# Performance work log

Hardware: AMD Instinct MI355X
Metric: run time of the kernel (lower is better)

The kernel has to match this reference:

```python
import jax, jax.numpy as jnp
import numpy as np

N_NODES = 100000
N_EDGES = 1600000
D_FEAT = 128
HIDDEN = 128
N_CLASSES = 40


def setup_inputs() -> dict:
    key = jax.random.key(0)
    ks = jax.random.split(key, 8)
    s = 1.0 / np.sqrt(HIDDEN)
    return {
        "x": jax.random.normal(ks[0], (N_NODES, D_FEAT), dtype=jnp.float32),
        "edge_index": jax.random.randint(ks[1], (2, N_EDGES), 0, N_NODES, dtype=jnp.int64),
        "w1a": jax.random.normal(ks[2], (D_FEAT, HIDDEN), dtype=jnp.float32) * s,
        "b1a": jnp.zeros((HIDDEN,), dtype=jnp.float32),
        "w1b": jax.random.normal(ks[3], (HIDDEN, HIDDEN), dtype=jnp.float32) * s,
        "b1b": jnp.zeros((HIDDEN,), dtype=jnp.float32),
        "w2a": jax.random.normal(ks[4], (HIDDEN, HIDDEN), dtype=jnp.float32) * s,
        "b2a": jnp.zeros((HIDDEN,), dtype=jnp.float32),
        "w2b": jax.random.normal(ks[5], (HIDDEN, HIDDEN), dtype=jnp.float32) * s,
        "b2b": jnp.zeros((HIDDEN,), dtype=jnp.float32),
        "wfc": jax.random.normal(ks[6], (HIDDEN, N_CLASSES), dtype=jnp.float32) * s,
        "bfc": jnp.zeros((N_CLASSES,), dtype=jnp.float32),
    }


def _gin_conv(x, src, dst, wa, ba, wb, bb):
    # sum-aggregate neighbor features: agg[i] = sum_{(j->i) in E} x[j]
    agg = jax.ops.segment_sum(x[src], dst, num_segments=N_NODES)
    h = x + agg  # eps = 0 (PyG GINConv default)
    h = jax.nn.relu(h @ wa + ba)
    return h @ wb + bb


def reference(x, edge_index, w1a, b1a, w1b, b1b, w2a, b2a, w2b, b2b, wfc, bfc):
    src, dst = edge_index[0], edge_index[1]
    h = jax.nn.relu(_gin_conv(x, src, dst, w1a, b1a, w1b, b1b))
    # dropout is identity at inference
    h = jax.nn.relu(_gin_conv(h, src, dst, w2a, b2a, w2b, b2b))
    logits = h @ wfc + bfc
    return jax.nn.log_softmax(logits, axis=1)
```

## Files before the change

kernel.cpp:

```cpp
#include <hip/hip_runtime.h>
#include <hip/hip_bf16.h>

#define NNODES 100000
#define NEDGES 1600000
#define DF 128
#define NC 40
#define NCP 48
#define NB 196
#define CH 4096
#define GEMM_BLOCKS 512
#define GEMM_WAVES (GEMM_BLOCKS * 4)
#define ZROW NNODES

typedef __bf16 bf16x8 __attribute__((ext_vector_type(8)));
typedef float f32x4 __attribute__((ext_vector_type(4)));
typedef float f32x2 __attribute__((ext_vector_type(2)));

__device__ __forceinline__ unsigned short f2bf(float f) {
    unsigned int u = __builtin_bit_cast(unsigned int, f);
    u = (u + 0x7FFFu + ((u >> 16) & 1u)) >> 16;
    return (unsigned short)u;
}
__device__ __forceinline__ float bf2f(unsigned short s) {
    unsigned int u = ((unsigned int)s) << 16;
    return __builtin_bit_cast(float, u);
}
__device__ __forceinline__ float bfLo(unsigned int u) {
    return __builtin_bit_cast(float, u << 16);
}
__device__ __forceinline__ float bfHi(unsigned int u) {
    return __builtin_bit_cast(float, u & 0xFFFF0000u);
}
__device__ __forceinline__ f32x2 up2(unsigned int u) {
    return (f32x2){bfLo(u), bfHi(u)};
}

__global__ void k_detect(const unsigned int* __restrict__ ei32,
                         const unsigned int* __restrict__ x32,
                         int* __restrict__ flags,
                         int* __restrict__ binCnt) {
    __shared__ unsigned int rOr[256];
    __shared__ int rCnt[256];
    for (int i = threadIdx.x; i < NB; i += 256) binCnt[i] = 0;
    unsigned int o = 0; int c = 0;
    for (int i = threadIdx.x; i < 1024; i += 256) o |= ei32[2 * i + 1];
    for (int i = threadIdx.x; i < 4096; i += 256) {
        unsigned int e = (x32[i] >> 7) & 0xFFu;
        c += (e >= 100u && e <= 140u) ? 1 : 0;
    }
    rOr[threadIdx.x] = o; rCnt[threadIdx.x] = c;
    __syncthreads();
    for (int s = 128; s; s >>= 1) {
        if ((int)threadIdx.x < s) {
            rOr[threadIdx.x] |= rOr[threadIdx.x + s];
            rCnt[threadIdx.x] += rCnt[threadIdx.x + s];
        }
        __syncthreads();
    }
    if (threadIdx.x == 0) {
        flags[0] = (rOr[0] == 0u) ? 1 : 0;
        flags[1] = (rCnt[0] > 2457) ? 1 : 0;
    }
}

__device__ __forceinline__ int ldIdx(const void* ei, int flag64, int i) {
    return flag64 ? (int)((const long long*)ei)[i] : ((const int*)ei)[i];
}

__global__ __launch_bounds__(256) void k_cvt_feat(const void* __restrict__ src,
                                                  const int* __restrict__ flags,
                                                  unsigned short* __restrict__ dst) {
    int i = blockIdx.x * 256 + threadIdx.x;
    if (flags[1]) {
        ((uint4*)dst)[i] = ((const uint4*)src)[i];
    } else {
        uint4 a = ((const uint4*)src)[2 * i];
        uint4 b = ((const uint4*)src)[2 * i + 1];
        auto pk = [](unsigned int lo, unsigned int hi) -> unsigned int {
            return ((unsigned int)f2bf(__builtin_bit_cast(float, hi)) << 16) |
                   f2bf(__builtin_bit_cast(float, lo));
        };
        uint4 r;
        r.x = pk(a.x, a.y);
        r.y = pk(a.z, a.w);
        r.z = pk(b.x, b.y);
        r.w = pk(b.z, b.w);
        ((uint4*)dst)[i] = r;
    }
}

__global__ __launch_bounds__(256) void k_wprep(const void* w1a, const void* w1b,
                                               const void* w2a, const void* w2b,
                                               const void* wfc,
                                               const void* b1a, const void* b1b,
                                               const void* b2a, const void* b2b,
                                               const void* bfc,
                                               const int* __restrict__ flags,
                                               unsigned short* __restrict__ wAll,
                                               float* __restrict__ bAll,
                                               unsigned short* __restrict__ pad0,
                                               unsigned short* __restrict__ pad1) {
    int idx = blockIdx.x * 256 + threadIdx.x;
    int bf = flags[1];
    auto ldf = [&](const void* p, int i) -> float {
        return bf ? bf2f(((const unsigned short*)p)[i]) : ((const float*)p)[i];
    };
    if (idx < 65536) {
        int wi = idx >> 14, r = idx & 16383;
        int n = r >> 7, k = r & 127;
        const void* s = (wi == 0) ? w1a : (wi == 1) ? w1b : (wi == 2) ? w2a : w2b;
        wAll[idx] = f2bf(ldf(s, k * 128 + n));
    } else if (idx < 65536 + NCP * 128) {
        int r = idx - 65536;
        int n = r >> 7, k = r & 127;
        wAll[idx] = (n < NC) ? f2bf(ldf(wfc, k * NC + n)) : (unsigned short)0;
    } else if (idx < 65536 + NCP * 128 + 512 + NC) {
        int r = idx - (65536 + NCP * 128);
        const void* s; int i;
        if (r < 128)      { s = b1a; i = r; }
        else if (r < 256) { s = b1b; i = r - 128; }
        else if (r < 384) { s = b2a; i = r - 256; }
        else if (r < 512) { s = b2b; i = r - 384; }
        else              { s = bfc; i = r - 512; }
        bAll[r] = ldf(s, i);
    } else if (idx < 65536 + NCP * 128 + 512 + NC + 256) {
        pad0[idx - (65536 + NCP * 128 + 512 + NC)] = 0;
    } else if (idx < 65536 + NCP * 128 + 512 + NC + 512) {
        pad1[idx - (65536 + NCP * 128 + 512 + NC + 256)] = 0;
    }
}

__global__ __launch_bounds__(256) void k_bincount(const void* __restrict__ ei,
                                                  const int* __restrict__ flags,
                                                  int* __restrict__ binCnt) {
    __shared__ int l[NB];
    int t = threadIdx.x;
    int f64 = flags[0];
    for (int i = t; i < NB; i += 256) l[i] = 0;
    __syncthreads();
    int base = blockIdx.x * CH;
#pragma unroll
    for (int k = 0; k < CH / 256; k++) {
        int e = base + k * 256 + t;
        if (e < NEDGES) atomicAdd(&l[ldIdx(ei, f64, NEDGES + e) >> 9], 1);
    }
    __syncthreads();
    for (int i = t; i < NB; i += 256)
        if (l[i]) atomicAdd(&binCnt[i], l[i]);
}

__global__ __launch_bounds__(256) void k_binscan(const int* __restrict__ binCnt,
                                                 int* __restrict__ binOfs,
                                                 int* __restrict__ binCur) {
    __shared__ int sh[256];
    int t = threadIdx.x;
    int v = (t < NB) ? binCnt[t] : 0;
    sh[t] = v;
    __syncthreads();
    for (int off = 1; off < 256; off <<= 1) {
        int x = (t >= off) ? sh[t - off] : 0;
        __syncthreads();
        sh[t] += x;
        __syncthreads();
    }
    if (t < NB) {
        binOfs[t + 1] = sh[t];
        binCur[t] = sh[t] - v;
    }
    if (t == 0) binOfs[0] = 0;
}

__global__ __launch_bounds__(256) void k_binscatter(const void* __restrict__ ei,
                                                    const int* __restrict__ flags,
                                                    int* __restrict__ binCur,
                                                    int2* __restrict__ ebin) {
    __shared__ int lcnt[NB], lbase[NB], lofs[NB];
    int t = threadIdx.x;
    int f64 = flags[0];
    for (int i = t; i < NB; i += 256) lcnt[i] = 0;
    __syncthreads();
    int base = blockIdx.x * CH;
    int2 ed[CH / 256];
    int bn[CH / 256];
#pragma unroll
    for (int k = 0; k < CH / 256; k++) {
        int e = base + k * 256 + t;
        if (e < NEDGES) {
            ed[k].x = ldIdx(ei, f64, e);
            ed[k].y = ldIdx(ei, f64, NEDGES + e);
            bn[k] = ed[k].y >> 9;
            atomicAdd(&lcnt[bn[k]], 1);
        } else bn[k] = -1;
    }
    __syncthreads();
    if (t < NB) {
        int c = lcnt[t];
        lbase[t] = c ? atomicAdd(&binCur[t], c) : 0;
        lofs[t] = 0;
    }
    __syncthreads();
#pragma unroll
    for (int k = 0; k < CH / 256; k++) {
        if (bn[k] >= 0) {
            int p = lbase[bn[k]] + atomicAdd(&lofs[bn[k]], 1);
            ebin[p] = ed[k];
        }
    }
}

__global__ __launch_bounds__(256) void k_binfill(const int2* __restrict__ ebin,
                                                 const int* __restrict__ binOfs,
                                                 int* __restrict__ rowptr,
                                                 int* __restrict__ perm) {
    __shared__ int deg[512], lptr[512], ssum[256];
    int b = blockIdx.x, t = threadIdx.x;
    int n0 = b << 9;
    int nn = NNODES - n0; if (nn > 512) nn = 512;
    int e0 = binOfs[b], e1 = binOfs[b + 1];
    deg[t] = 0; deg[t + 256] = 0;
    __syncthreads();
    for (int e = e0 + t; e < e1; e += 256)
        atomicAdd(&deg[ebin[e].y - n0], 1);
    __syncthreads();
    int d0 = deg[2 * t], d1 = deg[2 * t + 1];
    int s = d0 + d1;
    ssum[t] = s;
    __syncthreads();
    for (int off = 1; off < 256; off <<= 1) {
        int x = (t >= off) ? ssum[t - off] : 0;
        __syncthreads();
        ssum[t] += x;
        __syncthreads();
    }
    int ex = ssum[t] - s;
    lptr[2 * t] = ex;
    lptr[2 * t + 1] = ex + d0;
    if (2 * t < nn)     rowptr[n0 + 2 * t] = e0 + ex;
    if (2 * t + 1 < nn) rowptr[n0 + 2 * t + 1] = e0 + ex + d0;
    if (b == NB - 1 && t == 0) rowptr[NNODES] = e1;
    deg[2 * t] = 0; deg[2 * t + 1] = 0;
    __syncthreads();
    for (int e = e0 + t; e < e1; e += 256) {
        int2 ed = ebin[e];
        int d = ed.y - n0;
        int pos = e0 + lptr[d] + atomicAdd(&deg[d], 1);
        perm[pos] = ed.x;
    }
}

__device__ __forceinline__ void accu(f32x2* acc, uint4 u) {
    acc[0] += up2(u.x);
    acc[1] += up2(u.y);
    acc[2] += up2(u.z);
    acc[3] += up2(u.w);
}

template <int S>
__device__ __forceinline__ void gslots(const int* __restrict__ perm, const uint4* __restrict__ F,
                                       int j, int je, int g, int c, f32x2* acc) {
    int pm[S];
#pragma unroll
    for (int k = 0; k < S; k++) pm[k] = perm[j + 4 * k + g];
#pragma unroll
    for (int k = 0; k < S; k++)
        if (j + 4 * k + g >= je) pm[k] = ZROW;
    uint4 u[S];
#pragma unroll
    for (int k = 0; k < S; k++) u[k] = F[pm[k] * 16 + c];
#pragma unroll
    for (int k = 0; k < S; k++) accu(acc, u[k]);
}

__global__ __launch_bounds__(256) void k_gather(const unsigned short* __restrict__ feat,
                                                const unsigned short* __restrict__ x,
                                                const int* __restrict__ rowptr,
                                                const int* __restrict__ perm,
                                                unsigned short* __restrict__ out) {
    int wave = threadIdx.x >> 6, lane = threadIdx.x & 63;
    int i = blockIdx.x * 4 + wave;
    int g = lane >> 4, c = lane & 15;
    const uint4* F = (const uint4*)feat;

    uint4 xv = ((const uint4*)x)[i * 16 + c];
    int jb = rowptr[i], je = rowptr[i + 1];

    f32x2 acc[4];
#pragma unroll
    for (int k = 0; k < 4; k++) acc[k] = (f32x2){0.f, 0.f};

    int j = jb;
    while (je - j > 24) {
        int s0 = perm[j + g], s1 = perm[j + 4 + g];
        int s2 = perm[j + 8 + g], s3 = perm[j + 12 + g];
        uint4 u0 = F[s0 * 16 + c];
        uint4 u1 = F[s1 * 16 + c];
        uint4 u2 = F[s2 * 16 + c];
        uint4 u3 = F[s3 * 16 + c];
        accu(acc, u0); accu(acc, u1); accu(acc, u2); accu(acc, u3);
        j += 16;
    }
    int deg = je - j;
    if (deg > 16)      gslots<6>(perm, F, j, je, g, c, acc);
    else if (deg > 8)  gslots<4>(perm, F, j, je, g, c, acc);
    else if (deg > 0)  gslots<2>(perm, F, j, je, g, c, acc);

#pragma unroll
    for (int k = 0; k < 4; k++) {
        acc[k][0] += __shfl_xor(acc[k][0], 16);
        acc[k][1] += __shfl_xor(acc[k][1], 16);
        acc[k][0] += __shfl_xor(acc[k][0], 32);
        acc[k][1] += __shfl_xor(acc[k][1], 32);
    }

    acc[0] += up2(xv.x);
    acc[1] += up2(xv.y);
    acc[2] += up2(xv.z);
    acc[3] += up2(xv.w);

    if (g == 0) {
        uint4 r;
        r.x = ((unsigned int)f2bf(acc[0][1]) << 16) | f2bf(acc[0][0]);
        r.y = ((unsigned int)f2bf(acc[1][1]) << 16) | f2bf(acc[1][0]);
        r.z = ((unsigned int)f2bf(acc[2][1]) << 16) | f2bf(acc[2][0]);
        r.w = ((unsigned int)f2bf(acc[3][1]) << 16) | f2bf(acc[3][0]);
        ((uint4*)out)[i * 16 + c] = r;
    }
}

__global__ __launch_bounds__(256, 2) void k_gemm_rb(const unsigned short* __restrict__ A,
                                                    const unsigned short* __restrict__ WT,
                                                    const float* __restrict__ bias,
                                                    unsigned short* __restrict__ out) {
    int gw = blockIdx.x * 4 + (threadIdx.x >> 6);
    int lane = threadIdx.x & 63;
    int m = lane & 15, quad = lane >> 4;

    bf16x8 bfr[8][4];
#pragma unroll
    for (int nt = 0; nt < 8; nt++) {
        const unsigned short* Bb = WT + (nt * 16 + m) * DF + quad * 8;
#pragma unroll
        for (int ks = 0; ks < 4; ks++)
            bfr[nt][ks] = *(const bf16x8*)(Bb + ks * 32);
    }
    float bv[8];
#pragma unroll
    for (int nt = 0; nt < 8; nt++) bv[nt] = bias[nt * 16 + m];

    for (int tile = gw; tile < NNODES / 16; tile += GEMM_WAVES) {
        int r0 = tile * 16;
        const unsigned short* Ab = A + (r0 + m) * DF + quad * 8;
        bf16x8 a[4];
#pragma unroll
        for (int ks = 0; ks < 4; ks++) a[ks] = *(const bf16x8*)(Ab + ks * 32);

        f32x4 acc[8];
#pragma unroll
        for (int nt = 0; nt < 8; nt++) acc[nt] = (f32x4){0.f, 0.f, 0.f, 0.f};
#pragma unroll
        for (int nt = 0; nt < 8; nt++)
#pragma unroll
            for (int ks = 0; ks < 4; ks++)
                acc[nt] = __builtin_amdgcn_mfma_f32_16x16x32_bf16(a[ks], bfr[nt][ks], acc[nt], 0, 0, 0);

#pragma unroll
        for (int nt = 0; nt < 8; nt++) {
            int col = nt * 16 + m;
#pragma unroll
            for (int reg = 0; reg < 4; reg++) {
                int row = r0 + quad * 4 + reg;
                float v = acc[nt][reg] + bv[nt];
                if (v < 0.f) v = 0.f;
                out[row * DF + col] = f2bf(v);
            }
        }
    }
}

__global__ __launch_bounds__(256, 2) void k_fc_rb(const unsigned short* __restrict__ A,
                                                  const unsigned short* __restrict__ WfcT,
                                                  const float* __restrict__ bfc,
                                                  const int* __restrict__ flags,
                                                  void* __restrict__ out) {
    int gw = blockIdx.x * 4 + (threadIdx.x >> 6);
    int lane = threadIdx.x & 63;
    int m = lane & 15, quad = lane >> 4;
    bool valid2 = (m < 8);
    int obf = flags[1];

    bf16x8 bfr[3][4];
#pragma unroll
    for (int nt = 0; nt < 3; nt++) {
        const unsigned short* Bb = WfcT + (nt * 16 + m) * DF + quad * 8;
#pragma unroll
        for (int ks = 0; ks < 4; ks++)
            bfr[nt][ks] = *(const bf16x8*)(Bb + ks * 32);
    }
    float bv0 = bfc[m], bv1 = bfc[16 + m];
    float bv2 = valid2 ? bfc[32 + m] : 0.f;

    for (int tile = gw; tile < NNODES / 16; tile += GEMM_WAVES) {
        int r0 = tile * 16;
        const unsigned short* Ab = A + (r0 + m) * DF + quad * 8;
        bf16x8 a[4];
#pragma unroll
        for (int ks = 0; ks < 4; ks++) a[ks] = *(const bf16x8*)(Ab + ks * 32);

        f32x4 acc[3];
#pragma unroll
        for (int nt = 0; nt < 3; nt++) acc[nt] = (f32x4){0.f, 0.f, 0.f, 0.f};
#pragma unroll
        for (int nt = 0; nt < 3; nt++)
#pragma unroll
            for (int ks = 0; ks < 4; ks++)
                acc[nt] = __builtin_amdgcn_mfma_f32_16x16x32_bf16(a[ks], bfr[nt][ks], acc[nt], 0, 0, 0);

#pragma unroll
        for (int reg = 0; reg < 4; reg++) {
            float v0 = acc[0][reg] + bv0;
            float v1 = acc[1][reg] + bv1;
            float v2 = valid2 ? (acc[2][reg] + bv2) : -3.0e38f;
            float mx = fmaxf(fmaxf(v0, v1), v2);
#pragma unroll
            for (int off = 1; off < 16; off <<= 1) mx = fmaxf(mx, __shfl_xor(mx, off, 16));
            float e = __expf(v0 - mx) + __expf(v1 - mx) + (valid2 ? __expf(v2 - mx) : 0.f);
#pragma unroll
            for (int off = 1; off < 16; off <<= 1) e += __shfl_xor(e, off, 16);
            float l = mx + __logf(e);
            int row = r0 + quad * 4 + reg;
            if (obf) {
                unsigned short* o = (unsigned short*)out + row * NC;
                o[m] = f2bf(v0 - l);
                o[16 + m] = f2bf(v1 - l);
                if (valid2) o[32 + m] = f2bf(v2 - l);
            } else {
                float* o = (float*)out + row * NC;
                o[m] = v0 - l;
                o[16 + m] = v1 - l;
                if (valid2) o[32 + m] = v2 - l;
            }
        }
    }
}

extern "C" void kernel_launch(void* const* d_in, const int* in_sizes, int n_in,
                              void* d_out, int out_size, void* d_ws, size_t ws_size,
                              hipStream_t stream) {
    const void* x   = d_in[0];
    const void* ei  = d_in[1];
    const void* w1a = d_in[2];
    const void* b1a = d_in[3];
    const void* w1b = d_in[4];
    const void* b1b = d_in[5];
    const void* w2a = d_in[6];
    const void* b2a = d_in[7];
    const void* w2b = d_in[8];
    const void* b2b = d_in[9];
    const void* wfc = d_in[10];
    const void* bfc = d_in[11];

    char* ws = (char*)d_ws;
    size_t off = 0;
    auto alloc = [&](size_t bytes) {
        void* p = ws + off;
        off += (bytes + 255) & ~(size_t)255;
        return p;
    };
    unsigned short* B0    = (unsigned short*)alloc((size_t)(NNODES + 1) * DF * 2);
    unsigned short* B1    = (unsigned short*)alloc((size_t)(NNODES + 1) * DF * 2);
    unsigned short* B2    = (unsigned short*)alloc((size_t)NNODES * DF * 2);
    int2*           ebin  = (int2*)alloc((size_t)NEDGES * 8);
    int*            perm  = (int*)alloc((size_t)(NEDGES + 64) * 4);
    int*            rowptr= (int*)alloc((size_t)(NNODES + 1) * 4);
    int*            binCnt= (int*)alloc(NB * 4);
    int*            binOfs= (int*)alloc((NB + 1) * 4);
    int*            binCur= (int*)alloc(NB * 4);
    int*            flags = (int*)alloc(256);
    unsigned short* wAll  = (unsigned short*)alloc((4 * 16384 + NCP * 128) * 2);
    float*          bAll  = (float*)alloc((512 + NC) * 4);

    unsigned short* w1aT = wAll;
    unsigned short* w1bT = wAll + 16384;
    unsigned short* w2aT = wAll + 32768;
    unsigned short* w2bT = wAll + 49152;
    unsigned short* wfcT = wAll + 65536;
    float* b1af = bAll;
    float* b1bf = bAll + 128;
    float* b2af = bAll + 256;
    float* b2bf = bAll + 384;
    float* bfcf = bAll + 512;

    k_detect<<<1, 256, 0, stream>>>((const unsigned int*)ei, (const unsigned int*)x, flags, binCnt);
    k_cvt_feat<<<NNODES * DF / (256 * 8), 256, 0, stream>>>(x, flags, B0);

    int wprepN = 4 * 16384 + NCP * 128 + 512 + NC + 512;
    k_wprep<<<(wprepN + 255) / 256, 256, 0, stream>>>(w1a, w1b, w2a, w2b, wfc,
                                                      b1a, b1b, b2a, b2b, bfc,
                                                      flags, wAll, bAll,
                                                      B0 + (size_t)NNODES * DF,
                                                      B1 + (size_t)NNODES * DF);

    int nEB = (NEDGES + CH - 1) / CH;
    k_bincount<<<nEB, 256, 0, stream>>>(ei, flags, binCnt);
    k_binscan<<<1, 256, 0, stream>>>(binCnt, binOfs, binCur);
    k_binscatter<<<nEB, 256, 0, stream>>>(ei, flags, binCur, ebin);
    k_binfill<<<NB, 256, 0, stream>>>(ebin, binOfs, rowptr, perm);

    const int gatherGrid = NNODES / 4;

    k_gather<<<gatherGrid, 256, 0, stream>>>(B0, B0, rowptr, perm, B1);
    k_gemm_rb<<<GEMM_BLOCKS, 256, 0, stream>>>(B1, w1aT, b1af, B2);
    k_gemm_rb<<<GEMM_BLOCKS, 256, 0, stream>>>(B2, w1bT, b1bf, B1);

    k_gather<<<gatherGrid, 256, 0, stream>>>(B1, B1, rowptr, perm, B2);
    k_gemm_rb<<<GEMM_BLOCKS, 256, 0, stream>>>(B2, w2aT, b2af, B0);
    k_gemm_rb<<<GEMM_BLOCKS, 256, 0, stream>>>(B0, w2bT, b2bf, B2);

    k_fc_rb<<<GEMM_BLOCKS, 256, 0, stream>>>(B2, wfcT, bfcf, flags, d_out);
}
```

Measured before the change: 375.8 us.

## Fuse per-layer GIN MLP GEMMs and final FC/log-softmax into single kernels

Replaces the two separate GEMM kernels per GIN layer, plus the separate FC kernel, with one templated kernel that runs both MLP GEMMs per 16-row tile. The intermediate activation is staged through a swizzled per-wave LDS tile instead of global memory, and the second layer also folds in the FC and log-softmax. This removes intermediate HBM round-trips and three kernel launches. In exchange it doubles the weights held in registers (launch bounds drop to 1 block per CU, with half the grid), which lowers occupancy and latency hiding for the A-tile loads.

```diff
diff --git a/kernel.cpp b/kernel.cpp
--- a/kernel.cpp
+++ b/kernel.cpp
@@ -8,8 +8,8 @@
 #define NCP 48
 #define NB 196
 #define CH 4096
-#define GEMM_BLOCKS 512
-#define GEMM_WAVES (GEMM_BLOCKS * 4)
+#define MLP_BLOCKS 256
+#define MLP_WAVES (MLP_BLOCKS * 4)
 #define ZROW NNODES
 
 typedef __bf16 bf16x8 __attribute__((ext_vector_type(8)));
@@ -327,27 +327,60 @@
     }
 }
 
-__global__ __launch_bounds__(256, 2) void k_gemm_rb(const unsigned short* __restrict__ A,
-                                                    const unsigned short* __restrict__ WT,
-                                                    const float* __restrict__ bias,
-                                                    unsigned short* __restrict__ out) {
-    int gw = blockIdx.x * 4 + (threadIdx.x >> 6);
-    int lane = threadIdx.x & 63;
+template <bool DOFC>
+__global__ __launch_bounds__(256, 1) void k_mlp_rb(const unsigned short* __restrict__ A,
+                                                   const unsigned short* __restrict__ WaT,
+                                                   const float* __restrict__ ba,
+                                                   const unsigned short* __restrict__ WbT,
+                                                   const float* __restrict__ bb,
+                                                   const unsigned short* __restrict__ WfcT,
+                                                   const float* __restrict__ bfc,
+                                                   const int* __restrict__ flags,
+                                                   unsigned short* __restrict__ outH,
+                                                   void* __restrict__ outFC) {
+    __shared__ __align__(16) unsigned short smem[4 * 2176];
+    int wave = threadIdx.x >> 6, lane = threadIdx.x & 63;
+    int gw = blockIdx.x * 4 + wave;
     int m = lane & 15, quad = lane >> 4;
-
-    bf16x8 bfr[8][4];
+    unsigned short* T = smem + wave * 2176;
+
+    bf16x8 wa[8][4], wb[8][4];
 #pragma unroll
     for (int nt = 0; nt < 8; nt++) {
-        const unsigned short* Bb = WT + (nt * 16 + m) * DF + quad * 8;
-#pragma unroll
-        for (int ks = 0; ks < 4; ks++)
-            bfr[nt][ks] = *(const bf16x8*)(Bb + ks * 32);
-    }
-    float bv[8];
-#pragma unroll
-    for (int nt = 0; nt < 8; nt++) bv[nt] = bias[nt * 16 + m];
-
-    for (int tile = gw; tile < NNODES / 16; tile += GEMM_WAVES) {
+        const unsigned short* Ba = WaT + (nt * 16 + m) * DF + quad * 8;
+        const unsigned short* Bb = WbT + (nt * 16 + m) * DF + quad * 8;
+#pragma unroll
+        for (int ks = 0; ks < 4; ks++) {
+            wa[nt][ks] = *(const bf16x8*)(Ba + ks * 32);
+            wb[nt][ks] = *(const bf16x8*)(Bb + ks * 32);
+        }
+    }
+    float bva[8], bvb[8];
+#pragma unroll
+    for (int nt = 0; nt < 8; nt++) { bva[nt] = ba[nt * 16 + m]; bvb[nt] = bb[nt * 16 + m]; }
+
+    bf16x8 wf[3][4];
+    float fv0 = 0.f, fv1 = 0.f, fv2 = 0.f;
+    bool valid2 = (m < 8);
+    int obf = 0;
+    if (DOFC) {
+#pragma unroll
+        for (int nt = 0; nt < 3; nt++) {
+            const unsigned short* Bf = WfcT + (nt * 16 + m) * DF + quad * 8;
+#pragma unroll
+            for (int ks = 0; ks < 4; ks++) wf[nt][ks] = *(const bf16x8*)(Bf + ks * 32);
+        }
+        fv0 = bfc[m]; fv1 = bfc[16 + m];
+        fv2 = valid2 ? bfc[32 + m] : 0.f;
+        obf = flags[1];
+    }
+
+    auto ladr = [](int row, int col) -> int {
+        int chunk = (col >> 3) ^ ((row >> 3) << 2);
+        return row * 136 + chunk * 8 + (col & 7);
+    };
+
+    for (int tile = gw; tile < NNODES / 16; tile += MLP_WAVES) {
         int r0 = tile * 16;
         const unsigned short* Ab = A + (r0 + m) * DF + quad * 8;
         bf16x8 a[4];
@@ -361,83 +394,91 @@
         for (int nt = 0; nt < 8; nt++)
 #pragma unroll
             for (int ks = 0; ks < 4; ks++)
-                acc[nt] = __builtin_amdgcn_mfma_f32_16x16x32_bf16(a[ks], bfr[nt][ks], acc[nt], 0, 0, 0);
-
-#pragma unroll
-        for (int nt = 0; nt < 8; nt++) {
-            int col = nt * 16 + m;
+                acc[nt] = __builtin_amdgcn_mfma_f32_16x16x32_bf16(a[ks], wa[nt][ks], acc[nt], 0, 0, 0);
+
+#pragma unroll
+        for (int nt = 0; nt < 8; nt++)
 #pragma unroll
             for (int reg = 0; reg < 4; reg++) {
+                float v = acc[nt][reg] + bva[nt];
+                if (v < 0.f) v = 0.f;
+                T[ladr(quad * 4 + reg, nt * 16 + m)] = f2bf(v);
+            }
+
+        bf16x8 a2[4];
+#pragma unroll
+        for (int ks = 0; ks < 4; ks++) {
+            int chunk = (ks * 4 + quad) ^ ((m >> 3) << 2);
+            a2[ks] = *(const bf16x8*)&T[m * 136 + chunk * 8];
+        }
+#pragma unroll
+        for (int nt = 0; nt < 8; nt++) acc[nt] = (f32x4){0.f, 0.f, 0.f, 0.f};
+#pragma unroll
+        for (int nt = 0; nt < 8; nt++)
+#pragma unroll
+            for (int ks = 0; ks < 4; ks++)
+                acc[nt] = __builtin_amdgcn_mfma_f32_16x16x32_bf16(a2[ks], wb[nt][ks], acc[nt], 0, 0, 0);
+
+        if (!DOFC) {
+#pragma unroll
+            for (int nt = 0; nt < 8; nt++) {
+                int col = nt * 16 + m;
+#pragma unroll
+                for (int reg = 0; reg < 4; reg++) {
+                    int row = r0 + quad * 4 + reg;
+                    float v = acc[nt][reg] + bvb[nt];
+                    if (v < 0.f) v = 0.f;
+                    outH[row * DF + col] = f2bf(v);
+                }
+            }
+        } else {
+#pragma unroll
+            for (int nt = 0; nt < 8; nt++)
+#pragma unroll
+                for (int reg = 0; reg < 4; reg++) {
+                    float v = acc[nt][reg] + bvb[nt];
+                    if (v < 0.f) v = 0.f;
+                    T[ladr(quad * 4 + reg, nt * 16 + m)] = f2bf(v);
+                }
+            bf16x8 a3[4];
+#pragma unroll
+            for (int ks = 0; ks < 4; ks++) {
+                int chunk = (ks * 4 + quad) ^ ((m >> 3) << 2);
+                a3[ks] = *(const bf16x8*)&T[m * 136 + chunk * 8];
+            }
+            f32x4 fa[3];
+#pragma unroll
+            for (int nt = 0; nt < 3; nt++) fa[nt] = (f32x4){0.f, 0.f, 0.f, 0.f};
+#pragma unroll
+            for (int nt = 0; nt < 3; nt++)
+#pragma unroll
+                for (int ks = 0; ks < 4; ks++)
+                    fa[nt] = __builtin_amdgcn_mfma_f32_16x16x32_bf16(a3[ks], wf[nt][ks], fa[nt], 0, 0, 0);
+
+#pragma unroll
+            for (int reg = 0; reg < 4; reg++) {
+                float v0 = fa[0][reg] + fv0;
+                float v1 = fa[1][reg] + fv1;
+                float v2 = valid2 ? (fa[2][reg] + fv2) : -3.0e38f;
+                float mx = fmaxf(fmaxf(v0, v1), v2);
+#pragma unroll
+                for (int off = 1; off < 16; off <<= 1) mx = fmaxf(mx, __shfl_xor(mx, off, 16));
+                float e = __expf(v0 - mx) + __expf(v1 - mx) + (valid2 ? __expf(v2 - mx) : 0.f);
+#pragma unroll
+                for (int off = 1; off < 16; off <<= 1) e += __shfl_xor(e, off, 16);
+                float l = mx + __logf(e);
                 int row = r0 + quad * 4 + reg;
-                float v = acc[nt][reg] + bv[nt];
-                if (v < 0.f) v = 0.f;
-                out[row * DF + col] = f2bf(v);
-            }
-        }
-    }
-}
-
-__global__ __launch_bounds__(256, 2) void k_fc_rb(const unsigned short* __restrict__ A,
-                                                  const unsigned short* __restrict__ WfcT,
-                                                  const float* __restrict__ bfc,
-                                                  const int* __restrict__ flags,
-                                                  void* __restrict__ out) {
-    int gw = blockIdx.x * 4 + (threadIdx.x >> 6);
-    int lane = threadIdx.x & 63;
-    int m = lane & 15, quad = lane >> 4;
-    bool valid2 = (m < 8);
-    int obf = flags[1];
-
-    bf16x8 bfr[3][4];
-#pragma unroll
-    for (int nt = 0; nt < 3; nt++) {
-        const unsigned short* Bb = WfcT + (nt * 16 + m) * DF + quad * 8;
-#pragma unroll
-        for (int ks = 0; ks < 4; ks++)
-            bfr[nt][ks] = *(const bf16x8*)(Bb + ks * 32);
-    }
-    float bv0 = bfc[m], bv1 = bfc[16 + m];
-    float bv2 = valid2 ? bfc[32 + m] : 0.f;
-
-    for (int tile = gw; tile < NNODES / 16; tile += GEMM_WAVES) {
-        int r0 = tile * 16;
-        const unsigned short* Ab = A + (r0 + m) * DF + quad * 8;
-        bf16x8 a[4];
-#pragma unroll
-        for (int ks = 0; ks < 4; ks++) a[ks] = *(const bf16x8*)(Ab + ks * 32);
-
-        f32x4 acc[3];
-#pragma unroll
-        for (int nt = 0; nt < 3; nt++) acc[nt] = (f32x4){0.f, 0.f, 0.f, 0.f};
-#pragma unroll
-        for (int nt = 0; nt < 3; nt++)
-#pragma unroll
-            for (int ks = 0; ks < 4; ks++)
-                acc[nt] = __builtin_amdgcn_mfma_f32_16x16x32_bf16(a[ks], bfr[nt][ks], acc[nt], 0, 0, 0);
-
-#pragma unroll
-        for (int reg = 0; reg < 4; reg++) {
-            float v0 = acc[0][reg] + bv0;
-            float v1 = acc[1][reg] + bv1;
-            float v2 = valid2 ? (acc[2][reg] + bv2) : -3.0e38f;
-            float mx = fmaxf(fmaxf(v0, v1), v2);
-#pragma unroll
-            for (int off = 1; off < 16; off <<= 1) mx = fmaxf(mx, __shfl_xor(mx, off, 16));
-            float e = __expf(v0 - mx) + __expf(v1 - mx) + (valid2 ? __expf(v2 - mx) : 0.f);
-#pragma unroll
-            for (int off = 1; off < 16; off <<= 1) e += __shfl_xor(e, off, 16);
-            float l = mx + __logf(e);
-            int row = r0 + quad * 4 + reg;
-            if (obf) {
-                unsigned short* o = (unsigned short*)out + row * NC;
-                o[m] = f2bf(v0 - l);
-                o[16 + m] = f2bf(v1 - l);
-                if (valid2) o[32 + m] = f2bf(v2 - l);
-            } else {
-                float* o = (float*)out + row * NC;
-                o[m] = v0 - l;
-                o[16 + m] = v1 - l;
-                if (valid2) o[32 + m] = v2 - l;
+                if (obf) {
+                    unsigned short* o = (unsigned short*)outFC + row * NC;
+                    o[m] = f2bf(v0 - l);
+                    o[16 + m] = f2bf(v1 - l);
+                    if (valid2) o[32 + m] = f2bf(v2 - l);
+                } else {
+                    float* o = (float*)outFC + row * NC;
+                    o[m] = v0 - l;
+                    o[16 + m] = v1 - l;
+                    if (valid2) o[32 + m] = v2 - l;
+                }
             }
         }
     }
@@ -468,7 +509,6 @@
     };
     unsigned short* B0    = (unsigned short*)alloc((size_t)(NNODES + 1) * DF * 2);
     unsigned short* B1    = (unsigned short*)alloc((size_t)(NNODES + 1) * DF * 2);
-    unsigned short* B2    = (unsigned short*)alloc((size_t)NNODES * DF * 2);
     int2*           ebin  = (int2*)alloc((size_t)NEDGES * 8);
     int*            perm  = (int*)alloc((size_t)(NEDGES + 64) * 4);
     int*            rowptr= (int*)alloc((size_t)(NNODES + 1) * 4);
@@ -509,12 +549,10 @@
     const int gatherGrid = NNODES / 4;
 
     k_gather<<<gatherGrid, 256, 0, stream>>>(B0, B0, rowptr, perm, B1);
-    k_gemm_rb<<<GEMM_BLOCKS, 256, 0, stream>>>(B1, w1aT, b1af, B2);
-    k_gemm_rb<<<GEMM_BLOCKS, 256, 0, stream>>>(B2, w1bT, b1bf, B1);
-
-    k_gather<<<gatherGrid, 256, 0, stream>>>(B1, B1, rowptr, perm, B2);
-    k_gemm_rb<<<GEMM_BLOCKS, 256, 0, stream>>>(B2, w2aT, b2af, B0);
-    k_gemm_rb<<<GEMM_BLOCKS, 256, 0, stream>>>(B0, w2bT, b2bf, B2);
-
-    k_fc_rb<<<GEMM_BLOCKS, 256, 0, stream>>>(B2, wfcT, bfcf, flags, d_out);
-}
+    k_mlp_rb<false><<<MLP_BLOCKS, 256, 0, stream>>>(B1, w1aT, b1af, w1bT, b1bf,
+                                                    nullptr, nullptr, flags, B0, nullptr);
+
+    k_gather<<<gatherGrid, 256, 0, stream>>>(B0, B0, rowptr, perm, B1);
+    k_mlp_rb<true><<<MLP_BLOCKS, 256, 0, stream>>>(B1, w2aT, b2af, w2bT, b2bf,
+                                                   wfcT, bfcf, flags, nullptr, d_out);
+}
```

After: 367.1 us. 1.02x faster.
